# Kernel optimization log

Measured on AMD Instinct MI355X. Metric: run time of the kernel, lower is better.

The kernel has to match this reference:

```python
import jax, jax.numpy as jnp
import numpy as np

NUM_NODE_TYPES = 4
OUT_SHAPE = (3, 3)


def setup_inputs() -> dict:
    key = jax.random.key(0)
    k1, k2, k3, k4 = jax.random.split(key, 4)
    N, E, D = 100000, 1600000, 32
    x = jax.random.normal(k1, (N, D), dtype=jnp.float32)
    edge_index = jax.random.randint(k2, (2, E), 0, N, dtype=jnp.int64)
    node_types = jax.random.randint(k3, (N,), 0, NUM_NODE_TYPES, dtype=jnp.int64)
    # Linear weight: [out_features, in_features] = [prod(out_shape), 2*D + 2*num_node_types]
    W = jax.random.normal(k4, (int(np.prod(OUT_SHAPE)), 2 * D + 2 * NUM_NODE_TYPES), dtype=jnp.float32)
    return {"x": x, "edge_index": edge_index, "node_types": node_types, "W": W}


def reference(x, edge_index, node_types, W):
    src, dst = edge_index[0], edge_index[1]
    # Per-node one-hot type encodings [N, num_node_types]
    nt_oh = jax.nn.one_hot(node_types, NUM_NODE_TYPES, dtype=x.dtype)
    # Gather per-edge features and concat: [E, 2*D + 2*T]
    x_cat = jnp.concatenate([x[src], x[dst], nt_oh[src], nt_oh[dst]], axis=1)
    # Bias-free linear + tanh
    maps = jnp.tanh(jnp.einsum("ef,of->eo", x_cat, W))
    return maps.reshape(-1, OUT_SHAPE[0], OUT_SHAPE[1])
```

## Files before the change

kernel.cpp:

```cpp
#include <hip/hip_runtime.h>
#include <hip/hip_bf16.h>


#define ODIM 9
#define INF 72
#define PSTRIDE 12
#define TPB 256

__device__ __forceinline__ float fast_tanh(float v) {
    float e = __expf(2.0f * v);
    return 1.0f - 2.0f * __builtin_amdgcn_rcpf(e + 1.0f);
}

__global__ __launch_bounds__(TPB) void node_proj_kernel(
        const float* __restrict__ x, const int* __restrict__ nt,
        const float* __restrict__ W, float* __restrict__ Psrc,
        float* __restrict__ Pdst, int N) {
    int n = blockIdx.x * TPB + threadIdx.x;
    if (n >= N) return;
    float xv[32];
    const float4* xp = (const float4*)(x + (size_t)n * 32);
    #pragma unroll
    for (int i = 0; i < 8; ++i) {
        float4 r = xp[i];
        xv[4*i+0] = r.x; xv[4*i+1] = r.y; xv[4*i+2] = r.z; xv[4*i+3] = r.w;
    }
    int t = nt[n];
    float* ps = Psrc + (size_t)n * PSTRIDE;
    float* pd = Pdst + (size_t)n * PSTRIDE;
    #pragma unroll
    for (int o = 0; o < ODIM; ++o) {
        const float* wr = W + o * INF;
        float s1 = wr[64 + t];
        float s2 = wr[68 + t];
        #pragma unroll
        for (int f = 0; f < 32; ++f) {
            s1 += xv[f] * wr[f];
            s2 += xv[f] * wr[32 + f];
        }
        ps[o] = s1;
        pd[o] = s2;
    }
}

__global__ __launch_bounds__(TPB) void edge_kernel(
        const int* __restrict__ src, const int* __restrict__ dst,
        const float* __restrict__ Psrc, const float* __restrict__ Pdst,
        float* __restrict__ out, int E) {
    __shared__ __align__(16) float tile[TPB * ODIM];
    int e0 = blockIdx.x * TPB;
    int cnt = min(TPB, E - e0);
    int e = e0 + (int)threadIdx.x;
    if ((int)threadIdx.x < cnt) {
        int s = src[e];
        int d = dst[e];
        const float4* ps = (const float4*)(Psrc + (size_t)s * PSTRIDE);
        const float4* pd = (const float4*)(Pdst + (size_t)d * PSTRIDE);
        float4 a0 = ps[0], a1 = ps[1], a2 = ps[2];
        float4 b0 = pd[0], b1 = pd[1], b2 = pd[2];
        float v[ODIM] = {a0.x+b0.x, a0.y+b0.y, a0.z+b0.z, a0.w+b0.w,
                         a1.x+b1.x, a1.y+b1.y, a1.z+b1.z, a1.w+b1.w,
                         a2.x+b2.x};
        #pragma unroll
        for (int k = 0; k < ODIM; ++k)
            tile[threadIdx.x * ODIM + k] = fast_tanh(v[k]);
    }
    __syncthreads();
    if (cnt == TPB) {
        float4* o4 = (float4*)(out + (size_t)e0 * ODIM);
        const float4* t4 = (const float4*)tile;
        for (int i = threadIdx.x; i < TPB * ODIM / 4; i += TPB)
            o4[i] = t4[i];
    } else {
        for (int i = threadIdx.x; i < cnt * ODIM; i += TPB)
            out[(size_t)e0 * ODIM + i] = tile[i];
    }
}

__global__ __launch_bounds__(TPB) void edge_fused_kernel(
        const int* __restrict__ src, const int* __restrict__ dst,
        const float* __restrict__ x, const int* __restrict__ nt,
        const float* __restrict__ W, float* __restrict__ out, int E) {
    __shared__ __align__(16) float tile[TPB * ODIM];
    int e0 = blockIdx.x * TPB;
    int cnt = min(TPB, E - e0);
    int e = e0 + (int)threadIdx.x;
    if ((int)threadIdx.x < cnt) {
        int s = src[e];
        int d = dst[e];
        float xs[32], xd[32];
        const float4* xsp = (const float4*)(x + (size_t)s * 32);
        const float4* xdp = (const float4*)(x + (size_t)d * 32);
        #pragma unroll
        for (int i = 0; i < 8; ++i) {
            float4 rs = xsp[i], rd = xdp[i];
            xs[4*i+0]=rs.x; xs[4*i+1]=rs.y; xs[4*i+2]=rs.z; xs[4*i+3]=rs.w;
            xd[4*i+0]=rd.x; xd[4*i+1]=rd.y; xd[4*i+2]=rd.z; xd[4*i+3]=rd.w;
        }
        int ts = nt[s], td = nt[d];
        #pragma unroll
        for (int o = 0; o < ODIM; ++o) {
            const float* wr = W + o * INF;
            float acc = wr[64 + ts] + wr[68 + td];
            #pragma unroll
            for (int f = 0; f < 32; ++f)
                acc += xs[f] * wr[f] + xd[f] * wr[32 + f];
            tile[threadIdx.x * ODIM + o] = fast_tanh(acc);
        }
    }
    __syncthreads();
    if (cnt == TPB) {
        float4* o4 = (float4*)(out + (size_t)e0 * ODIM);
        const float4* t4 = (const float4*)tile;
        for (int i = threadIdx.x; i < TPB * ODIM / 4; i += TPB)
            o4[i] = t4[i];
    } else {
        for (int i = threadIdx.x; i < cnt * ODIM; i += TPB)
            out[(size_t)e0 * ODIM + i] = tile[i];
    }
}

extern "C" void kernel_launch(void* const* d_in, const int* in_sizes, int n_in,
                              void* d_out, int out_size, void* d_ws, size_t ws_size,
                              hipStream_t stream) {
    const float* x  = (const float*)d_in[0];
    const int*   ei = (const int*)d_in[1];
    const int*   nt = (const int*)d_in[2];
    const float* W  = (const float*)d_in[3];
    float* out = (float*)d_out;

    int N = in_sizes[2];
    int E = in_sizes[1] / 2;
    const int* src = ei;
    const int* dst = ei + E;

    size_t pbytes = (size_t)N * PSTRIDE * sizeof(float);
    if (ws_size >= 2 * pbytes) {
        float* Psrc = (float*)d_ws;
        float* Pdst = (float*)((char*)d_ws + pbytes);
        node_proj_kernel<<<(N + TPB - 1) / TPB, TPB, 0, stream>>>(x, nt, W, Psrc, Pdst, N);
        edge_kernel<<<(E + TPB - 1) / TPB, TPB, 0, stream>>>(src, dst, Psrc, Pdst, out, E);
    } else {
        edge_fused_kernel<<<(E + TPB - 1) / TPB, TPB, 0, stream>>>(src, dst, x, nt, W, out, E);
    }
}
```

Baseline: 140.5 us.

## Quantize node projections to int16 and split edge gather into src/dst passes

Node projections are stored as int16 fixed-point (scale 512) in 32-byte rows instead of fp32 rows. The edge stage is split into a src-gather pass that writes a compact per-edge intermediate, and a dst-gather pass that adds, dequantizes, applies tanh and writes the output with nontemporal stores. The intent is to shrink the gather footprint and improve cache locality of each random gather. In exchange it adds an intermediate buffer round trip, an extra launch, and quantization error.

```diff
diff --git a/kernel.cpp b/kernel.cpp
--- a/kernel.cpp
+++ b/kernel.cpp
@@ -1,11 +1,18 @@
 #include <hip/hip_runtime.h>
 #include <hip/hip_bf16.h>
+#include <hip/hip_fp16.h>
 
 
 #define ODIM 9
 #define INF 72
-#define PSTRIDE 12
+#define ROWB 32
+#define MIDW 5
 #define TPB 256
+#define QSCALE 512.0f
+#define QINV (1.0f / 512.0f)
+
+typedef unsigned int uint4n __attribute__((ext_vector_type(4)));
+typedef float float4n __attribute__((ext_vector_type(4)));
 
 __device__ __forceinline__ float fast_tanh(float v) {
     float e = __expf(2.0f * v);
@@ -14,20 +21,19 @@
 
 __global__ __launch_bounds__(TPB) void node_proj_kernel(
         const float* __restrict__ x, const int* __restrict__ nt,
-        const float* __restrict__ W, float* __restrict__ Psrc,
-        float* __restrict__ Pdst, int N) {
+        const float* __restrict__ W, char* __restrict__ Ps,
+        char* __restrict__ Pd, int N) {
     int n = blockIdx.x * TPB + threadIdx.x;
     if (n >= N) return;
     float xv[32];
-    const float4* xp = (const float4*)(x + (size_t)n * 32);
+    const float4n* xp = (const float4n*)(x + (size_t)n * 32);
     #pragma unroll
     for (int i = 0; i < 8; ++i) {
-        float4 r = xp[i];
+        float4n r = __builtin_nontemporal_load(xp + i);
         xv[4*i+0] = r.x; xv[4*i+1] = r.y; xv[4*i+2] = r.z; xv[4*i+3] = r.w;
     }
     int t = nt[n];
-    float* ps = Psrc + (size_t)n * PSTRIDE;
-    float* pd = Pdst + (size_t)n * PSTRIDE;
+    short qs[10], qd[10];
     #pragma unroll
     for (int o = 0; o < ODIM; ++o) {
         const float* wr = W + o * INF;
@@ -38,41 +44,96 @@
             s1 += xv[f] * wr[f];
             s2 += xv[f] * wr[32 + f];
         }
-        ps[o] = s1;
-        pd[o] = s2;
-    }
-}
-
-__global__ __launch_bounds__(TPB) void edge_kernel(
-        const int* __restrict__ src, const int* __restrict__ dst,
-        const float* __restrict__ Psrc, const float* __restrict__ Pdst,
-        float* __restrict__ out, int E) {
+        qs[o] = (short)__float2int_rn(s1 * QSCALE);
+        qd[o] = (short)__float2int_rn(s2 * QSCALE);
+    }
+    qs[9] = 0; qd[9] = 0;
+    union { short u[8]; uint4n v; } pk;
+    #pragma unroll
+    for (int i = 0; i < 8; ++i) pk.u[i] = qs[i];
+    *(uint4n*)(Ps + (size_t)n * ROWB) = pk.v;
+    *(unsigned int*)(Ps + (size_t)n * ROWB + 16) =
+        (unsigned int)(unsigned short)qs[8];
+    #pragma unroll
+    for (int i = 0; i < 8; ++i) pk.u[i] = qd[i];
+    *(uint4n*)(Pd + (size_t)n * ROWB) = pk.v;
+    *(unsigned int*)(Pd + (size_t)n * ROWB + 16) =
+        (unsigned int)(unsigned short)qd[8];
+}
+
+__global__ __launch_bounds__(TPB) void edge_src_kernel(
+        const int* __restrict__ src, const char* __restrict__ Ps,
+        unsigned int* __restrict__ mid, int E) {
+    __shared__ __align__(16) unsigned int stage[TPB * MIDW];
+    int e0 = blockIdx.x * TPB;
+    int cnt = min(TPB, E - e0);
+    int t = (int)threadIdx.x;
+    if (t < cnt) {
+        int s = __builtin_nontemporal_load(src + e0 + t);
+        uint4n a = *(const uint4n*)(Ps + (size_t)s * ROWB);
+        unsigned int b = *(const unsigned int*)(Ps + (size_t)s * ROWB + 16);
+        stage[t*MIDW+0] = a.x; stage[t*MIDW+1] = a.y;
+        stage[t*MIDW+2] = a.z; stage[t*MIDW+3] = a.w;
+        stage[t*MIDW+4] = b;
+    }
+    __syncthreads();
+    if (cnt == TPB) {
+        uint4n* m4 = (uint4n*)(mid + (size_t)e0 * MIDW);
+        const uint4n* s4 = (const uint4n*)stage;
+        for (int i = t; i < TPB * MIDW / 4; i += TPB)
+            __builtin_nontemporal_store(s4[i], m4 + i);
+    } else {
+        unsigned int* m = mid + (size_t)e0 * MIDW;
+        for (int i = t; i < cnt * MIDW; i += TPB) m[i] = stage[i];
+    }
+}
+
+__global__ __launch_bounds__(TPB) void edge_dst_kernel(
+        const int* __restrict__ dst, const char* __restrict__ Pd,
+        const unsigned int* __restrict__ mid, float* __restrict__ out, int E) {
+    __shared__ __align__(16) unsigned int mstage[TPB * MIDW];
     __shared__ __align__(16) float tile[TPB * ODIM];
     int e0 = blockIdx.x * TPB;
     int cnt = min(TPB, E - e0);
-    int e = e0 + (int)threadIdx.x;
-    if ((int)threadIdx.x < cnt) {
-        int s = src[e];
-        int d = dst[e];
-        const float4* ps = (const float4*)(Psrc + (size_t)s * PSTRIDE);
-        const float4* pd = (const float4*)(Pdst + (size_t)d * PSTRIDE);
-        float4 a0 = ps[0], a1 = ps[1], a2 = ps[2];
-        float4 b0 = pd[0], b1 = pd[1], b2 = pd[2];
-        float v[ODIM] = {a0.x+b0.x, a0.y+b0.y, a0.z+b0.z, a0.w+b0.w,
-                         a1.x+b1.x, a1.y+b1.y, a1.z+b1.z, a1.w+b1.w,
-                         a2.x+b2.x};
-        #pragma unroll
-        for (int k = 0; k < ODIM; ++k)
-            tile[threadIdx.x * ODIM + k] = fast_tanh(v[k]);
-    }
-    __syncthreads();
-    if (cnt == TPB) {
-        float4* o4 = (float4*)(out + (size_t)e0 * ODIM);
-        const float4* t4 = (const float4*)tile;
-        for (int i = threadIdx.x; i < TPB * ODIM / 4; i += TPB)
-            o4[i] = t4[i];
-    } else {
-        for (int i = threadIdx.x; i < cnt * ODIM; i += TPB)
+    int t = (int)threadIdx.x;
+    if (cnt == TPB) {
+        const uint4n* m4 = (const uint4n*)(mid + (size_t)e0 * MIDW);
+        uint4n* s4 = (uint4n*)mstage;
+        for (int i = t; i < TPB * MIDW / 4; i += TPB)
+            s4[i] = __builtin_nontemporal_load(m4 + i);
+    } else {
+        const unsigned int* m = mid + (size_t)e0 * MIDW;
+        for (int i = t; i < cnt * MIDW; i += TPB) mstage[i] = m[i];
+    }
+    __syncthreads();
+    if (t < cnt) {
+        int d = __builtin_nontemporal_load(dst + e0 + t);
+        uint4n a = *(const uint4n*)(Pd + (size_t)d * ROWB);
+        unsigned int b = *(const unsigned int*)(Pd + (size_t)d * ROWB + 16);
+        unsigned int gd[5] = {a.x, a.y, a.z, a.w, b};
+        #pragma unroll
+        for (int i = 0; i < 4; ++i) {
+            unsigned int ms = mstage[t*MIDW + i];
+            unsigned int gg = gd[i];
+            int s0 = (short)(ms & 0xffff), s1 = (short)(ms >> 16);
+            int d0 = (short)(gg & 0xffff), d1 = (short)(gg >> 16);
+            tile[t*ODIM + 2*i]     = fast_tanh((float)(s0 + d0) * QINV);
+            tile[t*ODIM + 2*i + 1] = fast_tanh((float)(s1 + d1) * QINV);
+        }
+        {
+            int s8 = (short)(mstage[t*MIDW + 4] & 0xffff);
+            int d8 = (short)(gd[4] & 0xffff);
+            tile[t*ODIM + 8] = fast_tanh((float)(s8 + d8) * QINV);
+        }
+    }
+    __syncthreads();
+    if (cnt == TPB) {
+        float4n* o4 = (float4n*)(out + (size_t)e0 * ODIM);
+        const float4n* t4 = (const float4n*)tile;
+        for (int i = t; i < TPB * ODIM / 4; i += TPB)
+            __builtin_nontemporal_store(t4[i], o4 + i);
+    } else {
+        for (int i = t; i < cnt * ODIM; i += TPB)
             out[(size_t)e0 * ODIM + i] = tile[i];
     }
 }
@@ -134,12 +195,15 @@
     const int* src = ei;
     const int* dst = ei + E;
 
-    size_t pbytes = (size_t)N * PSTRIDE * sizeof(float);
-    if (ws_size >= 2 * pbytes) {
-        float* Psrc = (float*)d_ws;
-        float* Pdst = (float*)((char*)d_ws + pbytes);
-        node_proj_kernel<<<(N + TPB - 1) / TPB, TPB, 0, stream>>>(x, nt, W, Psrc, Pdst, N);
-        edge_kernel<<<(E + TPB - 1) / TPB, TPB, 0, stream>>>(src, dst, Psrc, Pdst, out, E);
+    size_t tbl = (size_t)N * ROWB;
+    size_t midb = (size_t)E * MIDW * sizeof(unsigned int);
+    if (ws_size >= 2 * tbl + midb) {
+        char* Ps = (char*)d_ws;
+        char* Pd = Ps + tbl;
+        unsigned int* mid = (unsigned int*)(Pd + tbl);
+        node_proj_kernel<<<(N + TPB - 1) / TPB, TPB, 0, stream>>>(x, nt, W, Ps, Pd, N);
+        edge_src_kernel<<<(E + TPB - 1) / TPB, TPB, 0, stream>>>(src, Ps, mid, E);
+        edge_dst_kernel<<<(E + TPB - 1) / TPB, TPB, 0, stream>>>(dst, Pd, mid, out, E);
     } else {
         edge_fused_kernel<<<(E + TPB - 1) / TPB, TPB, 0, stream>>>(src, dst, x, nt, W, out, E);
     }
```

After: 129.9 us. 7.6% less time.
